# Kernel tuning notes

Measured on AMD Instinct MI355X. Metric: run time of the kernel, lower is better.

Reference implementation:

```python
import jax, jax.numpy as jnp
import numpy as np

N_NODES = 100000
N_EDGES = 1600000
N_GRAPHS = 64
IN_DIM, HID, NCLS = 128, 256, 16


def setup_inputs() -> dict:
    key = jax.random.key(0)
    ks = jax.random.split(key, 8)
    x = jax.random.normal(ks[0], (N_NODES, IN_DIM), dtype=jnp.float32)
    src = jax.random.randint(ks[1], (N_EDGES,), 0, N_NODES, dtype=jnp.int32)
    dst = jax.random.randint(ks[2], (N_EDGES,), 0, N_NODES, dtype=jnp.int32)
    graph_ids = jnp.sort(jax.random.randint(ks[3], (N_NODES,), 0, N_GRAPHS, dtype=jnp.int32))
    W = jax.random.normal(ks[4], (IN_DIM, HID), dtype=jnp.float32) * 0.05
    b = jax.random.normal(ks[5], (HID,), dtype=jnp.float32) * 0.05
    Wc = jax.random.normal(ks[6], (HID, NCLS), dtype=jnp.float32) * 0.05
    bc = jax.random.normal(ks[7], (NCLS,), dtype=jnp.float32) * 0.05
    return {"x": x, "src": src, "dst": dst, "graph_ids": graph_ids,
            "W": W, "b": b, "Wc": Wc, "bc": bc}


def reference(x, src, dst, graph_ids, W, b, Wc, bc):
    ones = jnp.ones((src.shape[0],), dtype=x.dtype)
    # degrees on the graph WITH self-loops (dgl.add_self_loop adds +1 each)
    deg_out = jax.ops.segment_sum(ones, src, num_segments=N_NODES) + 1.0
    deg_in = jax.ops.segment_sum(ones, dst, num_segments=N_NODES) + 1.0
    norm_src = jax.lax.rsqrt(deg_out)[:, None]  # D_out^{-1/2}
    norm_dst = jax.lax.rsqrt(deg_in)[:, None]   # D_in^{-1/2}
    xs = x * norm_src
    # SpMM aggregation (sum over incoming edges) + self-loop contribution
    agg = jax.ops.segment_sum(xs[src], dst, num_segments=N_NODES) + xs
    h = agg * norm_dst
    # GraphConv linear (bias=True default), then ReLU
    h = jax.nn.relu(h @ W + b)
    # dgl.max_nodes: per-graph max pooling over nodes
    hg = jax.ops.segment_max(h, graph_ids, num_segments=N_GRAPHS)
    logits = hg @ Wc + bc
    return jax.nn.log_softmax(logits, axis=1)
```

## Files before the change

### kernel.cpp

```cpp
#include <hip/hip_runtime.h>
#include <hip/hip_bf16.h>
#include <math.h>

#define N_NODES 100000
#define N_EDGES 1600000
#define N_GRAPHS 64
#define IN_DIM 128
#define HID 256
#define NCLS 16

#define SCAN_CHUNK 1024
#define SCAN_BLOCKS ((N_NODES + SCAN_CHUNK - 1) / SCAN_CHUNK)

#define NREG 8
#define REGSZ (N_NODES / NREG)
#define NSLC 32
#define SLICE (N_EDGES / NSLC)

__global__ __launch_bounds__(256) void k_deghist(
    const int* __restrict__ src, const int* __restrict__ dst,
    int* __restrict__ scratch) {
  __shared__ int hist[REGSZ];
  int slice = blockIdx.x, region = blockIdx.y, z = blockIdx.z;
  const int* arr = z ? src : dst;
  int t = threadIdx.x;
  for (int r = t; r < REGSZ; r += 256) hist[r] = 0;
  __syncthreads();
  int base = region * REGSZ;
  const int4* a4 = (const int4*)(arr + (size_t)slice * SLICE);
  for (int i = t; i < SLICE / 4; i += 256) {
    int4 v = a4[i];
    int d;
    d = v.x - base; if ((unsigned)d < REGSZ) atomicAdd(&hist[d], 1);
    d = v.y - base; if ((unsigned)d < REGSZ) atomicAdd(&hist[d], 1);
    d = v.z - base; if ((unsigned)d < REGSZ) atomicAdd(&hist[d], 1);
    d = v.w - base; if ((unsigned)d < REGSZ) atomicAdd(&hist[d], 1);
  }
  __syncthreads();
  int* outp = scratch + ((size_t)(z * NREG + region) * NSLC + slice) * REGSZ;
  for (int r = t; r < REGSZ; r += 256) outp[r] = hist[r];
}

__global__ void k_degreduce(const int* __restrict__ scratch,
                            int* __restrict__ deg_in, int* __restrict__ deg_out) {
  int i = blockIdx.x * blockDim.x + threadIdx.x;
  if (i >= 2 * N_NODES) return;
  int z = i / N_NODES;
  int node = i - z * N_NODES;
  int region = node / REGSZ;
  int r = node - region * REGSZ;
  const int* p = scratch + (size_t)(z * NREG + region) * NSLC * REGSZ + r;
  int s = 0;
#pragma unroll
  for (int sl = 0; sl < NSLC; sl++) s += p[(size_t)sl * REGSZ];
  if (z == 0) deg_in[node] = s; else deg_out[node] = s;
}

__global__ void k_scan1(const int* __restrict__ deg_in, int* __restrict__ offs,
                        int* __restrict__ blockSums) {
  __shared__ int sdata[256];
  int b = blockIdx.x, t = threadIdx.x;
  int base = b * SCAN_CHUNK + t * 4;
  int v[4];
#pragma unroll
  for (int j = 0; j < 4; j++) {
    int idx = base + j;
    v[j] = (idx < N_NODES) ? deg_in[idx] : 0;
  }
  int tsum = v[0] + v[1] + v[2] + v[3];
  sdata[t] = tsum;
  __syncthreads();
  for (int off = 1; off < 256; off <<= 1) {
    int x = sdata[t];
    int y = (t >= off) ? sdata[t - off] : 0;
    __syncthreads();
    sdata[t] = x + y;
    __syncthreads();
  }
  int run = sdata[t] - tsum;
#pragma unroll
  for (int j = 0; j < 4; j++) {
    int idx = base + j;
    if (idx < N_NODES) offs[idx] = run;
    run += v[j];
  }
  if (t == 255) blockSums[b] = sdata[255];
}

__global__ void k_scan2(int* __restrict__ blockSums) {
  __shared__ int sdata[128];
  int t = threadIdx.x;
  int v = (t < SCAN_BLOCKS) ? blockSums[t] : 0;
  sdata[t] = v;
  __syncthreads();
  for (int off = 1; off < 128; off <<= 1) {
    int x = sdata[t];
    int y = (t >= off) ? sdata[t - off] : 0;
    __syncthreads();
    sdata[t] = x + y;
    __syncthreads();
  }
  if (t < SCAN_BLOCKS) blockSums[t] = sdata[t] - v;
}

__global__ void k_finalize(const int* __restrict__ deg_out, const int* __restrict__ deg_in,
                           const int* __restrict__ blockSums,
                           int* __restrict__ offs, int* __restrict__ cursor,
                           float* __restrict__ norm_src, float* __restrict__ norm_dst) {
  int i = blockIdx.x * blockDim.x + threadIdx.x;
  if (i >= N_NODES) return;
  int o = offs[i] + blockSums[i / SCAN_CHUNK];
  offs[i] = o;
  cursor[i] = o;
  norm_src[i] = rsqrtf((float)deg_out[i] + 1.0f);
  norm_dst[i] = rsqrtf((float)deg_in[i] + 1.0f);
}

__global__ void k_premul(const float* __restrict__ x, const float* __restrict__ norm_src,
                         __hip_bfloat162* __restrict__ xs) {
  int i = blockIdx.x * blockDim.x + threadIdx.x;
  if (i >= N_NODES * (IN_DIM / 2)) return;
  int v = i >> 6;
  float ns = norm_src[v];
  float2 a = ((const float2*)x)[i];
  __hip_bfloat162 o;
  o.x = __float2bfloat16(a.x * ns);
  o.y = __float2bfloat16(a.y * ns);
  xs[i] = o;
}

#define SC_SLICES 256
#define SC_CHUNK (N_EDGES / SC_SLICES)
#define SC_REGION (N_NODES / 8)
__global__ __launch_bounds__(256) void k_scatter(
    const int* __restrict__ src, const int* __restrict__ dst,
    int* __restrict__ cursor, int* __restrict__ edge_src) {
  int slice = blockIdx.x >> 3;
  int region = blockIdx.x & 7;
  int base = slice * SC_CHUNK;
  for (int i = threadIdx.x; i < SC_CHUNK; i += 256) {
    int e = base + i;
    int d = dst[e];
    if (d / SC_REGION == region) {
      int pos = atomicAdd(&cursor[d], 1);
      edge_src[pos] = src[e];
    }
  }
}

__global__ __launch_bounds__(256) void k_aggregate(
    const __hip_bfloat162* __restrict__ xs, const int* __restrict__ edge_src,
    const int* __restrict__ offs, const int* __restrict__ deg_in,
    const float* __restrict__ norm_dst, float* __restrict__ agg) {
  int wave = (blockIdx.x * blockDim.x + threadIdx.x) >> 6;
  int lane = threadIdx.x & 63;
  if (wave >= N_NODES) return;
  int v = wave;
  __hip_bfloat162 a = xs[(size_t)v * 64 + lane];
  float accx = __bfloat162float(a.x), accy = __bfloat162float(a.y);
  int beg = offs[v];
  int deg = deg_in[v];
  int e = beg;
  int end8 = beg + (deg & ~7);
  for (; e < end8; e += 8) {
    int u0 = edge_src[e + 0], u1 = edge_src[e + 1];
    int u2 = edge_src[e + 2], u3 = edge_src[e + 3];
    int u4 = edge_src[e + 4], u5 = edge_src[e + 5];
    int u6 = edge_src[e + 6], u7 = edge_src[e + 7];
    __hip_bfloat162 x0 = xs[(size_t)u0 * 64 + lane];
    __hip_bfloat162 x1 = xs[(size_t)u1 * 64 + lane];
    __hip_bfloat162 x2 = xs[(size_t)u2 * 64 + lane];
    __hip_bfloat162 x3 = xs[(size_t)u3 * 64 + lane];
    __hip_bfloat162 x4 = xs[(size_t)u4 * 64 + lane];
    __hip_bfloat162 x5 = xs[(size_t)u5 * 64 + lane];
    __hip_bfloat162 x6 = xs[(size_t)u6 * 64 + lane];
    __hip_bfloat162 x7 = xs[(size_t)u7 * 64 + lane];
    accx += __bfloat162float(x0.x) + __bfloat162float(x1.x) +
            __bfloat162float(x2.x) + __bfloat162float(x3.x) +
            __bfloat162float(x4.x) + __bfloat162float(x5.x) +
            __bfloat162float(x6.x) + __bfloat162float(x7.x);
    accy += __bfloat162float(x0.y) + __bfloat162float(x1.y) +
            __bfloat162float(x2.y) + __bfloat162float(x3.y) +
            __bfloat162float(x4.y) + __bfloat162float(x5.y) +
            __bfloat162float(x6.y) + __bfloat162float(x7.y);
  }
  int end = beg + deg;
  for (; e < end; e++) {
    int u = edge_src[e];
    __hip_bfloat162 xu = xs[(size_t)u * 64 + lane];
    accx += __bfloat162float(xu.x);
    accy += __bfloat162float(xu.y);
  }
  float nd = norm_dst[v];
  float2 outv;
  outv.x = accx * nd;
  outv.y = accy * nd;
  ((float2*)(agg + (size_t)v * IN_DIM))[lane] = outv;
}

__global__ __launch_bounds__(256) void k_aggregate_f32(
    const float* __restrict__ x, const int* __restrict__ edge_src,
    const int* __restrict__ offs, const int* __restrict__ deg_in,
    const float* __restrict__ norm_src, const float* __restrict__ norm_dst,
    float* __restrict__ agg) {
  int wave = (blockIdx.x * blockDim.x + threadIdx.x) >> 6;
  int lane = threadIdx.x & 63;
  if (wave >= N_NODES) return;
  int v = wave;
  float2 a = ((const float2*)(x + (size_t)v * IN_DIM))[lane];
  float ns = norm_src[v];
  float accx = a.x * ns, accy = a.y * ns;
  int beg = offs[v];
  int deg = deg_in[v];
  for (int e = beg; e < beg + deg; e++) {
    int u = edge_src[e];
    float nu = norm_src[u];
    float2 xu = ((const float2*)(x + (size_t)u * IN_DIM))[lane];
    accx += xu.x * nu;
    accy += xu.y * nu;
  }
  float nd = norm_dst[v];
  float2 outv;
  outv.x = accx * nd;
  outv.y = accy * nd;
  ((float2*)(agg + (size_t)v * IN_DIM))[lane] = outv;
}

#define BM 128
#define BN 128
#define BK 32
#define LDT 132

__global__ __launch_bounds__(256, 4) void k_gemm_pool(
    const float* __restrict__ agg, const float* __restrict__ W,
    const float* __restrict__ bias, const int* __restrict__ graph_ids,
    float* __restrict__ hg) {
  __shared__ float As[BK][LDT];
  __shared__ float Bs[BK][LDT];
  __shared__ float red[4][BN];

  int r0 = blockIdx.x * BM;
  int c0 = blockIdx.y * BN;
  int t = threadIdx.x;
  int tx = t & 15;
  int ty = t >> 4;

  float acc[8][8];
#pragma unroll
  for (int i = 0; i < 8; i++)
#pragma unroll
    for (int j = 0; j < 8; j++) acc[i][j] = 0.f;

  for (int kp = 0; kp < IN_DIM; kp += BK) {
    {
      int kq = (t & 7) << 2;
      int row = t >> 3;
#pragma unroll
      for (int it = 0; it < 4; it++) {
        int rl = row + it * 32;
        int grow = r0 + rl;
        int srow = grow < N_NODES ? grow : N_NODES - 1;
        float4 vv = *(const float4*)&agg[(size_t)srow * IN_DIM + kp + kq];
        As[kq + 0][rl] = vv.x;
        As[kq + 1][rl] = vv.y;
        As[kq + 2][rl] = vv.z;
        As[kq + 3][rl] = vv.w;
      }
    }
    {
      int cc = (t & 31) << 2;
      int kk = t >> 5;
#pragma unroll
      for (int it = 0; it < 4; it++) {
        int kl = kk + it * 8;
        float4 vv = *(const float4*)&W[(size_t)(kp + kl) * HID + c0 + cc];
        *(float4*)&Bs[kl][cc] = vv;
      }
    }
    __syncthreads();

#pragma unroll 2
    for (int kk = 0; kk < BK; kk++) {
      float4 a0 = *(float4*)&As[kk][ty * 4];
      float4 a1 = *(float4*)&As[kk][64 + ty * 4];
      float4 b0 = *(float4*)&Bs[kk][tx * 4];
      float4 b1 = *(float4*)&Bs[kk][64 + tx * 4];
      float av[8] = {a0.x, a0.y, a0.z, a0.w, a1.x, a1.y, a1.z, a1.w};
      float bv[8] = {b0.x, b0.y, b0.z, b0.w, b1.x, b1.y, b1.z, b1.w};
#pragma unroll
      for (int i = 0; i < 8; i++)
#pragma unroll
        for (int j = 0; j < 8; j++) acc[i][j] += av[i] * bv[j];
    }
    __syncthreads();
  }

  float bias_v[8];
#pragma unroll
  for (int j = 0; j < 8; j++) {
    int c = c0 + ((j < 4) ? (tx * 4 + j) : (64 + tx * 4 + j - 4));
    bias_v[j] = bias[c];
  }
  int gid[8];
#pragma unroll
  for (int i = 0; i < 8; i++) {
    int r = r0 + ((i < 4) ? (ty * 4 + i) : (64 + ty * 4 + i - 4));
    gid[i] = (r < N_NODES) ? graph_ids[r] : -1;
  }
#pragma unroll
  for (int i = 0; i < 8; i++)
#pragma unroll
    for (int j = 0; j < 8; j++) acc[i][j] = fmaxf(acc[i][j] + bias_v[j], 0.f);

  int gmin = graph_ids[r0];
  int rlast = r0 + BM - 1;
  if (rlast >= N_NODES) rlast = N_NODES - 1;
  int gmax = graph_ids[rlast];
  int w = t >> 6;

  for (int g = gmin; g <= gmax; g++) {
    float m[8];
#pragma unroll
    for (int j = 0; j < 8; j++) m[j] = 0.f;
#pragma unroll
    for (int i = 0; i < 8; i++) {
      if (gid[i] == g) {
#pragma unroll
        for (int j = 0; j < 8; j++) m[j] = fmaxf(m[j], acc[i][j]);
      }
    }
#pragma unroll
    for (int j = 0; j < 8; j++) {
      m[j] = fmaxf(m[j], __shfl_xor(m[j], 16, 64));
      m[j] = fmaxf(m[j], __shfl_xor(m[j], 32, 64));
    }
    if ((t & 63) < 16) {
#pragma unroll
      for (int j = 0; j < 8; j++) {
        int cl = (j < 4) ? (tx * 4 + j) : (64 + tx * 4 + j - 4);
        red[w][cl] = m[j];
      }
    }
    __syncthreads();
    if (t < BN) {
      float mm = fmaxf(fmaxf(red[0][t], red[1][t]), fmaxf(red[2][t], red[3][t]));
      atomicMax((unsigned int*)&hg[g * HID + c0 + t], __float_as_uint(mm));
    }
    __syncthreads();
  }
}

__global__ void k_classify(const float* __restrict__ hg, const float* __restrict__ Wc,
                           const float* __restrict__ bc, float* __restrict__ out) {
  int g = threadIdx.x;
  if (g >= N_GRAPHS) return;
  float logits[NCLS];
#pragma unroll
  for (int c = 0; c < NCLS; c++) logits[c] = bc[c];
  for (int k = 0; k < HID; k++) {
    float h = hg[g * HID + k];
#pragma unroll
    for (int c = 0; c < NCLS; c++) logits[c] += h * Wc[k * NCLS + c];
  }
  float m = logits[0];
#pragma unroll
  for (int c = 1; c < NCLS; c++) m = fmaxf(m, logits[c]);
  float s = 0.f;
#pragma unroll
  for (int c = 0; c < NCLS; c++) s += expf(logits[c] - m);
  float lse = logf(s) + m;
#pragma unroll
  for (int c = 0; c < NCLS; c++) out[g * NCLS + c] = logits[c] - lse;
}

extern "C" void kernel_launch(void* const* d_in, const int* in_sizes, int n_in,
                              void* d_out, int out_size, void* d_ws, size_t ws_size,
                              hipStream_t stream) {
  const float* x = (const float*)d_in[0];
  const int* src = (const int*)d_in[1];
  const int* dst = (const int*)d_in[2];
  const int* graph_ids = (const int*)d_in[3];
  const float* W = (const float*)d_in[4];
  const float* b = (const float*)d_in[5];
  const float* Wc = (const float*)d_in[6];
  const float* bc = (const float*)d_in[7];
  float* out = (float*)d_out;

  int* deg_out = (int*)d_ws;
  int* deg_in = deg_out + N_NODES;
  float* hg = (float*)(deg_in + N_NODES);
  float* norm_src = hg + N_GRAPHS * HID;
  float* norm_dst = norm_src + N_NODES;
  int* offs = (int*)(norm_dst + N_NODES);
  int* cursor = offs + N_NODES;
  int* blockSums = cursor + N_NODES;
  int* edge_src = blockSums + 128;
  float* agg = (float*)(edge_src + N_EDGES);
  __hip_bfloat162* xs = (__hip_bfloat162*)(agg + (size_t)N_NODES * IN_DIM);
  size_t need = (char*)(xs + (size_t)N_NODES * (IN_DIM / 2)) - (char*)d_ws;
  bool use_bf16 = ws_size >= need;
  int* deg_scratch = (int*)agg;

  size_t zbytes = (size_t)(2 * N_NODES + N_GRAPHS * HID) * 4;
  hipMemsetAsync(d_ws, 0, zbytes, stream);

  k_deghist<<<dim3(NSLC, NREG, 2), 256, 0, stream>>>(src, dst, deg_scratch);
  k_degreduce<<<(2 * N_NODES + 255) / 256, 256, 0, stream>>>(deg_scratch, deg_in, deg_out);
  k_scan1<<<SCAN_BLOCKS, 256, 0, stream>>>(deg_in, offs, blockSums);
  k_scan2<<<1, 128, 0, stream>>>(blockSums);
  k_finalize<<<(N_NODES + 255) / 256, 256, 0, stream>>>(deg_out, deg_in, blockSums,
                                                        offs, cursor, norm_src, norm_dst);
  if (use_bf16)
    k_premul<<<(N_NODES * (IN_DIM / 2) + 255) / 256, 256, 0, stream>>>(x, norm_src, xs);
  k_scatter<<<2048, 256, 0, stream>>>(src, dst, cursor, edge_src);
  if (use_bf16)
    k_aggregate<<<N_NODES / 4, 256, 0, stream>>>(xs, edge_src, offs, deg_in,
                                                 norm_dst, agg);
  else
    k_aggregate_f32<<<N_NODES / 4, 256, 0, stream>>>(x, edge_src, offs, deg_in,
                                                     norm_src, norm_dst, agg);
  dim3 ggrid((N_NODES + BM - 1) / BM, HID / BN);
  k_gemm_pool<<<ggrid, 256, 0, stream>>>(agg, W, b, graph_ids, hg);
  k_classify<<<1, 64, 0, stream>>>(hg, Wc, bc, out);
}
```

Baseline: 411.2 us.

## Use bf16 MFMA with hi/lo split for fused GEMM+max-pool

```diff
diff --git a/kernel.cpp b/kernel.cpp
--- a/kernel.cpp
+++ b/kernel.cpp
@@ -11,6 +11,18 @@
 
 #define SCAN_CHUNK 1024
 #define SCAN_BLOCKS ((N_NODES + SCAN_CHUNK - 1) / SCAN_CHUNK)
+
+typedef __attribute__((ext_vector_type(8))) short short8v;
+typedef __attribute__((ext_vector_type(4))) float f32x4;
+
+__device__ __forceinline__ unsigned short bf16_rne(float f) {
+  unsigned int u = __float_as_uint(f);
+  u += 0x7fffu + ((u >> 16) & 1u);
+  return (unsigned short)(u >> 16);
+}
+__device__ __forceinline__ float bf16_to_f32(unsigned short h) {
+  return __uint_as_float(((unsigned int)h) << 16);
+}
 
 #define NREG 8
 #define REGSZ (N_NODES / NREG)
@@ -127,6 +139,14 @@
   o.x = __float2bfloat16(a.x * ns);
   o.y = __float2bfloat16(a.y * ns);
   xs[i] = o;
+}
+
+__global__ void k_prepW(const float* __restrict__ W, unsigned short* __restrict__ Wt) {
+  int i = blockIdx.x * blockDim.x + threadIdx.x;
+  if (i >= HID * IN_DIM) return;
+  int n = i >> 7;
+  int k = i & 127;
+  Wt[n * IN_DIM + k] = bf16_rne(W[(size_t)k * HID + n]);
 }
 
 #define SC_SLICES 256
@@ -226,123 +246,108 @@
   ((float2*)(agg + (size_t)v * IN_DIM))[lane] = outv;
 }
 
-#define BM 128
-#define BN 128
-#define BK 32
-#define LDT 132
+#define GBM 128
+#define GBN 128
 
 __global__ __launch_bounds__(256, 4) void k_gemm_pool(
-    const float* __restrict__ agg, const float* __restrict__ W,
+    const float* __restrict__ agg, const unsigned short* __restrict__ Wt,
     const float* __restrict__ bias, const int* __restrict__ graph_ids,
     float* __restrict__ hg) {
-  __shared__ float As[BK][LDT];
-  __shared__ float Bs[BK][LDT];
-  __shared__ float red[4][BN];
-
-  int r0 = blockIdx.x * BM;
-  int c0 = blockIdx.y * BN;
+  __shared__ float red[4][GBN];
+
+  int r0 = blockIdx.x * GBM;
+  int c0 = blockIdx.y * GBN;
   int t = threadIdx.x;
-  int tx = t & 15;
-  int ty = t >> 4;
-
-  float acc[8][8];
-#pragma unroll
-  for (int i = 0; i < 8; i++)
-#pragma unroll
-    for (int j = 0; j < 8; j++) acc[i][j] = 0.f;
-
-  for (int kp = 0; kp < IN_DIM; kp += BK) {
-    {
-      int kq = (t & 7) << 2;
-      int row = t >> 3;
-#pragma unroll
-      for (int it = 0; it < 4; it++) {
-        int rl = row + it * 32;
-        int grow = r0 + rl;
-        int srow = grow < N_NODES ? grow : N_NODES - 1;
-        float4 vv = *(const float4*)&agg[(size_t)srow * IN_DIM + kp + kq];
-        As[kq + 0][rl] = vv.x;
-        As[kq + 1][rl] = vv.y;
-        As[kq + 2][rl] = vv.z;
-        As[kq + 3][rl] = vv.w;
+  int w = t >> 6;
+  int lane = t & 63;
+  int lg = lane >> 4;
+  int li = lane & 15;
+  int m_wave = r0 + w * 32;
+
+  f32x4 acc[2][8];
+#pragma unroll
+  for (int tm = 0; tm < 2; tm++)
+#pragma unroll
+    for (int tn = 0; tn < 8; tn++) acc[tm][tn] = (f32x4){0.f, 0.f, 0.f, 0.f};
+
+#pragma unroll 1
+  for (int kp = 0; kp < IN_DIM; kp += 32) {
+    short8v ah[2], al[2];
+#pragma unroll
+    for (int tm = 0; tm < 2; tm++) {
+      int row = m_wave + tm * 16 + li;
+      int srow = row < N_NODES ? row : N_NODES - 1;
+      const float* p = agg + (size_t)srow * IN_DIM + kp + lg * 8;
+      float4 v0 = *(const float4*)p;
+      float4 v1 = *(const float4*)(p + 4);
+      float fa[8] = {v0.x, v0.y, v0.z, v0.w, v1.x, v1.y, v1.z, v1.w};
+#pragma unroll
+      for (int j = 0; j < 8; j++) {
+        unsigned short h = bf16_rne(fa[j]);
+        ah[tm][j] = (short)h;
+        al[tm][j] = (short)bf16_rne(fa[j] - bf16_to_f32(h));
       }
     }
-    {
-      int cc = (t & 31) << 2;
-      int kk = t >> 5;
-#pragma unroll
-      for (int it = 0; it < 4; it++) {
-        int kl = kk + it * 8;
-        float4 vv = *(const float4*)&W[(size_t)(kp + kl) * HID + c0 + cc];
-        *(float4*)&Bs[kl][cc] = vv;
+#pragma unroll
+    for (int tn = 0; tn < 8; tn++) {
+      int ncol = c0 + tn * 16 + li;
+      short8v b = *(const short8v*)(Wt + (size_t)ncol * IN_DIM + kp + lg * 8);
+#pragma unroll
+      for (int tm = 0; tm < 2; tm++) {
+        acc[tm][tn] = __builtin_amdgcn_mfma_f32_16x16x32_bf16(al[tm], b, acc[tm][tn], 0, 0, 0);
+        acc[tm][tn] = __builtin_amdgcn_mfma_f32_16x16x32_bf16(ah[tm], b, acc[tm][tn], 0, 0, 0);
       }
     }
-    __syncthreads();
-
-#pragma unroll 2
-    for (int kk = 0; kk < BK; kk++) {
-      float4 a0 = *(float4*)&As[kk][ty * 4];
-      float4 a1 = *(float4*)&As[kk][64 + ty * 4];
-      float4 b0 = *(float4*)&Bs[kk][tx * 4];
-      float4 b1 = *(float4*)&Bs[kk][64 + tx * 4];
-      float av[8] = {a0.x, a0.y, a0.z, a0.w, a1.x, a1.y, a1.z, a1.w};
-      float bv[8] = {b0.x, b0.y, b0.z, b0.w, b1.x, b1.y, b1.z, b1.w};
-#pragma unroll
-      for (int i = 0; i < 8; i++)
-#pragma unroll
-        for (int j = 0; j < 8; j++) acc[i][j] += av[i] * bv[j];
-    }
-    __syncthreads();
   }
 
   float bias_v[8];
 #pragma unroll
-  for (int j = 0; j < 8; j++) {
-    int c = c0 + ((j < 4) ? (tx * 4 + j) : (64 + tx * 4 + j - 4));
-    bias_v[j] = bias[c];
-  }
+  for (int tn = 0; tn < 8; tn++) bias_v[tn] = bias[c0 + tn * 16 + li];
   int gid[8];
 #pragma unroll
-  for (int i = 0; i < 8; i++) {
-    int r = r0 + ((i < 4) ? (ty * 4 + i) : (64 + ty * 4 + i - 4));
-    gid[i] = (r < N_NODES) ? graph_ids[r] : -1;
-  }
-#pragma unroll
-  for (int i = 0; i < 8; i++)
-#pragma unroll
-    for (int j = 0; j < 8; j++) acc[i][j] = fmaxf(acc[i][j] + bias_v[j], 0.f);
+  for (int tm = 0; tm < 2; tm++)
+#pragma unroll
+    for (int reg = 0; reg < 4; reg++) {
+      int r = m_wave + tm * 16 + lg * 4 + reg;
+      gid[tm * 4 + reg] = (r < N_NODES) ? graph_ids[r] : -1;
+    }
+#pragma unroll
+  for (int tm = 0; tm < 2; tm++)
+#pragma unroll
+    for (int tn = 0; tn < 8; tn++)
+#pragma unroll
+      for (int reg = 0; reg < 4; reg++)
+        acc[tm][tn][reg] = fmaxf(acc[tm][tn][reg] + bias_v[tn], 0.f);
 
   int gmin = graph_ids[r0];
-  int rlast = r0 + BM - 1;
+  int rlast = r0 + GBM - 1;
   if (rlast >= N_NODES) rlast = N_NODES - 1;
   int gmax = graph_ids[rlast];
-  int w = t >> 6;
 
   for (int g = gmin; g <= gmax; g++) {
     float m[8];
 #pragma unroll
-    for (int j = 0; j < 8; j++) m[j] = 0.f;
-#pragma unroll
-    for (int i = 0; i < 8; i++) {
-      if (gid[i] == g) {
-#pragma unroll
-        for (int j = 0; j < 8; j++) m[j] = fmaxf(m[j], acc[i][j]);
+    for (int tn = 0; tn < 8; tn++) m[tn] = 0.f;
+#pragma unroll
+    for (int tm = 0; tm < 2; tm++)
+#pragma unroll
+      for (int reg = 0; reg < 4; reg++) {
+        if (gid[tm * 4 + reg] == g) {
+#pragma unroll
+          for (int tn = 0; tn < 8; tn++) m[tn] = fmaxf(m[tn], acc[tm][tn][reg]);
+        }
       }
-    }
-#pragma unroll
-    for (int j = 0; j < 8; j++) {
-      m[j] = fmaxf(m[j], __shfl_xor(m[j], 16, 64));
-      m[j] = fmaxf(m[j], __shfl_xor(m[j], 32, 64));
-    }
-    if ((t & 63) < 16) {
-#pragma unroll
-      for (int j = 0; j < 8; j++) {
-        int cl = (j < 4) ? (tx * 4 + j) : (64 + tx * 4 + j - 4);
-        red[w][cl] = m[j];
-      }
-    }
-    __syncthreads();
-    if (t < BN) {
+#pragma unroll
+    for (int tn = 0; tn < 8; tn++) {
+      m[tn] = fmaxf(m[tn], __shfl_xor(m[tn], 16, 64));
+      m[tn] = fmaxf(m[tn], __shfl_xor(m[tn], 32, 64));
+    }
+    if (lane < 16) {
+#pragma unroll
+      for (int tn = 0; tn < 8; tn++) red[w][tn * 16 + li] = m[tn];
+    }
+    __syncthreads();
+    if (t < GBN) {
       float mm = fmaxf(fmaxf(red[0][t], red[1][t]), fmaxf(red[2][t], red[3][t]));
       atomicMax((unsigned int*)&hg[g * HID + c0 + t], __float_as_uint(mm));
     }
@@ -395,7 +400,8 @@
   int* cursor = offs + N_NODES;
   int* blockSums = cursor + N_NODES;
   int* edge_src = blockSums + 128;
-  float* agg = (float*)(edge_src + N_EDGES);
+  unsigned short* Wt = (unsigned short*)(edge_src + N_EDGES);
+  float* agg = (float*)(Wt + HID * IN_DIM);
   __hip_bfloat162* xs = (__hip_bfloat162*)(agg + (size_t)N_NODES * IN_DIM);
   size_t need = (char*)(xs + (size_t)N_NODES * (IN_DIM / 2)) - (char*)d_ws;
   bool use_bf16 = ws_size >= need;
@@ -404,6 +410,7 @@
   size_t zbytes = (size_t)(2 * N_NODES + N_GRAPHS * HID) * 4;
   hipMemsetAsync(d_ws, 0, zbytes, stream);
 
+  k_prepW<<<(HID * IN_DIM + 255) / 256, 256, 0, stream>>>(W, Wt);
   k_deghist<<<dim3(NSLC, NREG, 2), 256, 0, stream>>>(src, dst, deg_scratch);
   k_degreduce<<<(2 * N_NODES + 255) / 256, 256, 0, stream>>>(deg_scratch, deg_in, deg_out);
   k_scan1<<<SCAN_BLOCKS, 256, 0, stream>>>(deg_in, offs, blockSums);
@@ -419,7 +426,7 @@
   else
     k_aggregate_f32<<<N_NODES / 4, 256, 0, stream>>>(x, edge_src, offs, deg_in,
                                                      norm_src, norm_dst, agg);
-  dim3 ggrid((N_NODES + BM - 1) / BM, HID / BN);
-  k_gemm_pool<<<ggrid, 256, 0, stream>>>(agg, W, b, graph_ids, hg);
+  dim3 ggrid((N_NODES + GBM - 1) / GBM, HID / GBN);
+  k_gemm_pool<<<ggrid, 256, 0, stream>>>(agg, Wt, b, graph_ids, hg);
   k_classify<<<1, 64, 0, stream>>>(hg, Wc, bc, out);
 }
```

After: 383.1 us. 6.8% less time.
